# Kernel optimization log

Measured on AMD Instinct MI355X. Metric: run time of the kernel, lower is better.

Reference implementation:

```python
import jax, jax.numpy as jnp
import numpy as np

# ---- neuron / simulation params (network.yaml analogue) ----
THETA = 10.0      # spike threshold
TAU_SR = 4.0      # SRM (psp) kernel time constant
TAU_REF = 4.0     # refractory kernel time constant
SCALE_REF = 2.0
TS = 1.0          # simulation step
T_SAMPLE = 1000
N_BATCH, N_IN, N_OUT = 16, 2048, 512
SPIKE_RATE = 0.1


def _alpha_kernel(tau, mult, eps_cut):
    # SLAYER _calculateAlphaKernel: truncated alpha function samples
    vals = []
    for t in np.arange(0.0, T_SAMPLE, TS):
        v = mult * t / tau * np.exp(1.0 - t / tau)
        if abs(v) < eps_cut and t > tau:
            break
        vals.append(v)
    return np.asarray(vals, dtype=np.float32)

SRM_KERNEL = _alpha_kernel(TAU_SR, 1.0, 0.01)
REF_KERNEL = _alpha_kernel(TAU_REF, -SCALE_REF * THETA, 0.0001)  # fullRefKernel=True
# pending-refractory shift vector: refKernel[0]==0 is consumed at spike time
REF_SHIFT = jnp.asarray(np.concatenate([REF_KERNEL[1:], [0.0]]).astype(np.float32))


def psp(spike_in):
    # causal temporal filter: psp[n,c,t] = Ts * sum_j srm[j] * s[n,c,t-j]
    N, C, T = spike_in.shape
    Ls = SRM_KERNEL.shape[0]
    x = spike_in.reshape(N * C, 1, T)
    k = jnp.asarray(SRM_KERNEL)[::-1].reshape(1, 1, Ls)  # flip -> convolution
    y = jax.lax.conv_general_dilated(
        x, k, window_strides=(1,), padding=[(Ls - 1, 0)],
        dimension_numbers=('NCH', 'OIH', 'NCH'))
    return y.reshape(N, C, T) * TS


def spike_scan(wpsp):
    # sequential spike generation with refractory feedback (SLAYER getSpikes)
    N, C, T = wpsp.shape
    L = REF_SHIFT.shape[0]

    def step(buf, x):
        u = x + buf[..., 0]                       # membrane incl. past refractory
        ind = (u >= THETA).astype(x.dtype)
        buf = jnp.concatenate([buf[..., 1:], jnp.zeros_like(buf[..., :1])], -1) \
              + ind[..., None] * REF_SHIFT        # schedule refractory for future t
        return buf, (ind / TS, u)

    buf0 = jnp.zeros((N, C, L), wpsp.dtype)
    _, (s, u) = jax.lax.scan(step, buf0, jnp.moveaxis(wpsp, -1, 0))
    return jnp.moveaxis(s, 0, -1), jnp.moveaxis(u, 0, -1)


def setup_inputs() -> dict:
    key = jax.random.key(0)
    k1, k2 = jax.random.split(key)
    spikeInput = (jax.random.uniform(k1, (N_BATCH, N_IN, T_SAMPLE)) < SPIKE_RATE
                  ).astype(jnp.float32)
    weight = jax.random.normal(k2, (N_OUT, N_IN), dtype=jnp.float32) * 0.3
    return {'spikeInput': spikeInput, 'weight': weight}


def reference(spikeInput, weight):
    p = psp(spikeInput)                           # [N, Nin, T]
    wpsp = jnp.einsum('oi,nit->not', weight, p)   # 1x1x1 conv == matmul, no bias
    spikes, _ = spike_scan(wpsp)                  # [N, Nout, T]
    return spikes
```

## Files before the change

kernel.cpp:

```cpp
#include <hip/hip_runtime.h>
#include <hip/hip_bf16.h>
#include <math.h>

#define NB 16
#define NIN 2048
#define NOUT 512
#define TT 1000
#define L_SRM 31

typedef int v4i  __attribute__((ext_vector_type(4)));
typedef int v16i __attribute__((ext_vector_type(16)));

__device__ __forceinline__ unsigned long long spread8(unsigned int b) {
    unsigned long long x = (unsigned long long)(b & 0xFFu) * 0x0101010101010101ULL;
    x &= 0x8040201008040201ULL;
    x |= x >> 4; x |= x >> 2; x |= x >> 1;
    return x & 0x0101010101010101ULL;
}

__global__ __launch_bounds__(256) void k_quant(const float* __restrict__ W,
                                               signed char* __restrict__ Bq) {
    int idx = blockIdx.x * 256 + threadIdx.x;
    int o = idx >> 11, i = idx & (NIN - 1);
    double w = (double)W[o * NIN + i];
    int wq = (int)rint(w * 536870912.0);
    int b0 = (int)(signed char)(wq & 255); int r = (wq - b0) >> 8;
    int b1 = (int)(signed char)(r  & 255); r = (r - b1) >> 8;
    int b2 = (int)(signed char)(r  & 255); r = (r - b2) >> 8;
    int b3 = r;
    size_t e = (size_t)o * NIN + i;
    Bq[e]                = (signed char)b0;
    Bq[e + 1048576]      = (signed char)b1;
    Bq[e + 2097152]      = (signed char)b2;
    Bq[e + 3145728]      = (signed char)b3;
}

__global__ __launch_bounds__(256) void k_extract(const float* __restrict__ s,
                                                 unsigned long long* __restrict__ bits) {
    __shared__ float tile[64][65];
    int tc = blockIdx.x, ic = blockIdx.y, n = blockIdx.z;
    int t0 = tc * 64, i0 = ic * 64;
    int tid = threadIdx.x;
    int r = tid >> 2, cq = tid & 3;
    const float* rp = s + ((size_t)(n * NIN + i0 + r)) * TT + t0;
    #pragma unroll
    for (int q = 0; q < 4; ++q) {
        int col = cq * 16 + q * 4;
        float4 v = make_float4(0.f, 0.f, 0.f, 0.f);
        if (t0 + col + 3 < TT) v = *(const float4*)(rp + col);
        tile[r][col] = v.x; tile[r][col + 1] = v.y;
        tile[r][col + 2] = v.z; tile[r][col + 3] = v.w;
    }
    __syncthreads();
    int lane = tid & 63, w = tid >> 6;
    #pragma unroll
    for (int k = 0; k < 16; ++k) {
        int tl = w * 16 + k;
        if (t0 + tl >= TT) break;
        unsigned long long m = __ballot(tile[lane][tl] != 0.0f);
        if (lane == 0) bits[((size_t)n * TT + t0 + tl) * 32 + ic] = m;
    }
}

__global__ __launch_bounds__(512) void k_spmm(const unsigned long long* __restrict__ bits,
                                              const signed char* __restrict__ Bq,
                                              double* __restrict__ z) {
    __shared__ char Alds[128 * 128];
    __shared__ char Blds[4][64 * 128];
    int tid = threadIdx.x;
    int bid = blockIdx.x;
    int o0  = (bid & 7) * 64;
    int nt0 = (bid >> 3) * 128;

    const int arow_w = tid >> 2, q = tid & 3;
    const int p_st = tid >> 7, orow = (tid >> 1) & 63, h = tid & 1;
    const unsigned int* agp = (const unsigned int*)bits + (size_t)(nt0 + arow_w) * 64 + q;
    const signed char*  bgp = Bq + (size_t)p_st * (NOUT * NIN)
                                 + (size_t)(o0 + orow) * NIN + h * 64;
    char* awp = Alds + arow_w * 128;
    const int xra_w = arow_w & 7;
    char* bwp = Blds[p_st] + orow * 128;
    const int xro_w = orow & 7;

    const int l = tid & 63, wv = tid >> 6;
    const int wm = wv >> 1, wn = wv & 1;
    const int arow = wm * 32 + (l & 31), xra = arow & 7;
    const int brow = wn * 32 + (l & 31), xrb = brow & 7;
    const int kg = l >> 5;

    v16i acc0 = {}, acc1 = {}, acc2 = {}, acc3 = {};

    unsigned int aw = agp[0];
    int4 bs0 = ((const int4*)bgp)[0], bs1 = ((const int4*)bgp)[1],
         bs2 = ((const int4*)bgp)[2], bs3 = ((const int4*)bgp)[3];

    for (int ks = 0; ks < 16; ++ks) {
        __syncthreads();
        {
            unsigned long long s0 = spread8(aw), s1 = spread8(aw >> 8),
                               s2 = spread8(aw >> 16), s3 = spread8(aw >> 24);
            ulonglong2 v0; v0.x = s0; v0.y = s1;
            ulonglong2 v1; v1.x = s2; v1.y = s3;
            *(ulonglong2*)(awp + (((2 * q)     ^ xra_w) << 4)) = v0;
            *(ulonglong2*)(awp + (((2 * q + 1) ^ xra_w) << 4)) = v1;
            *(int4*)(bwp + (((h * 4 + 0) ^ xro_w) << 4)) = bs0;
            *(int4*)(bwp + (((h * 4 + 1) ^ xro_w) << 4)) = bs1;
            *(int4*)(bwp + (((h * 4 + 2) ^ xro_w) << 4)) = bs2;
            *(int4*)(bwp + (((h * 4 + 3) ^ xro_w) << 4)) = bs3;
        }
        __syncthreads();
        if (ks < 15) {
            aw = agp[(ks + 1) * 4];
            const int4* g = (const int4*)(bgp + (size_t)(ks + 1) * 128);
            bs0 = g[0]; bs1 = g[1]; bs2 = g[2]; bs3 = g[3];
        }
        #pragma unroll
        for (int ksub = 0; ksub < 4; ++ksub) {
            int ca = ksub * 2 + kg;
            v4i av  = *(const v4i*)(Alds    + arow * 128 + (((ca) ^ xra) << 4));
            v4i bv0 = *(const v4i*)(Blds[0] + brow * 128 + (((ca) ^ xrb) << 4));
            v4i bv1 = *(const v4i*)(Blds[1] + brow * 128 + (((ca) ^ xrb) << 4));
            v4i bv2 = *(const v4i*)(Blds[2] + brow * 128 + (((ca) ^ xrb) << 4));
            v4i bv3 = *(const v4i*)(Blds[3] + brow * 128 + (((ca) ^ xrb) << 4));
            acc0 = __builtin_amdgcn_mfma_i32_32x32x32_i8(av, bv0, acc0, 0, 0, 0);
            acc1 = __builtin_amdgcn_mfma_i32_32x32x32_i8(av, bv1, acc1, 0, 0, 0);
            acc2 = __builtin_amdgcn_mfma_i32_32x32x32_i8(av, bv2, acc2, 0, 0, 0);
            acc3 = __builtin_amdgcn_mfma_i32_32x32x32_i8(av, bv3, acc3, 0, 0, 0);
        }
    }

    #pragma unroll
    for (int r = 0; r < 16; ++r) {
        int row = (r & 3) + 8 * (r >> 2) + 4 * kg;
        long long tot = ((long long)acc3[r] << 24) + ((long long)acc2[r] << 16)
                      + ((long long)acc1[r] << 8)  +  (long long)acc0[r];
        double zv = (double)tot * (1.0 / 536870912.0);
        __builtin_nontemporal_store(zv,
            &z[(size_t)(nt0 + wm * 32 + row) * NOUT + (o0 + wn * 32 + (l & 31))]);
    }
}

__global__ __launch_bounds__(128) void k_conv(const double* __restrict__ z,
                                              double* __restrict__ wpsp) {
    __shared__ float srm_s[32];
    __shared__ __align__(16) double zs[62 * 128];
    int tid = threadIdx.x;
    if (tid < L_SRM) {
        double t = (double)tid;
        srm_s[tid] = (float)((t / 4.0) * exp(1.0 - t / 4.0));
    }
    int tb = blockIdx.x * 32;
    int oc = blockIdx.y * 128;
    int n  = blockIdx.z;
    const double* zp = z + ((size_t)n * TT) * NOUT + oc;
    int wv = tid >> 6, lane = tid & 63;
    for (int r = wv; r < 62; r += 2) {
        int t = tb - 30 + r;
        if (t >= 0 && t < TT) {
            const double* src = zp + (size_t)t * NOUT + lane * 2;
            __builtin_amdgcn_global_load_lds(
                (const __attribute__((address_space(1))) void*)src,
                (__attribute__((address_space(3))) void*)(&zs[r * 128]),
                16, 0, 0);
        } else {
            double2 zero; zero.x = 0.0; zero.y = 0.0;
            *(double2*)(&zs[r * 128 + lane * 2]) = zero;
        }
    }
    asm volatile("s_waitcnt vmcnt(0)" ::: "memory");
    __syncthreads();
    for (int tl = 0; tl < 32; ++tl) {
        int t = tb + tl;
        if (t >= TT) break;
        double a0 = 0., a1 = 0., a2 = 0., a3 = 0.;
        #pragma unroll
        for (int jj = 0; jj < 28; jj += 4) {
            a0 += (double)srm_s[jj]     * zs[(tl + 30 - jj) * 128 + tid];
            a1 += (double)srm_s[jj + 1] * zs[(tl + 29 - jj) * 128 + tid];
            a2 += (double)srm_s[jj + 2] * zs[(tl + 28 - jj) * 128 + tid];
            a3 += (double)srm_s[jj + 3] * zs[(tl + 27 - jj) * 128 + tid];
        }
        a0 += (double)srm_s[28] * zs[(tl + 2) * 128 + tid];
        a1 += (double)srm_s[29] * zs[(tl + 1) * 128 + tid];
        a2 += (double)srm_s[30] * zs[(tl + 0) * 128 + tid];
        wpsp[((size_t)n * TT + t) * NOUT + oc + tid] = (a0 + a1) + (a2 + a3);
    }
}

__global__ __launch_bounds__(64) void k_scan(const double* __restrict__ wpsp,
                                             float* __restrict__ out) {
    __shared__ float  refTab[64];
    __shared__ double Tb[8][256];
    __shared__ __align__(16) double xbuf[2][34 * 64];
    __shared__ float  obuf[64 * 33];
    int lane = threadIdx.x;
    {
        double d = (double)lane;
        refTab[lane] = (lane == 0) ? 0.0f
                     : (float)(-20.0 * (d / 4.0) * exp(1.0 - d / 4.0));
    }
    __syncthreads();
    for (int e = lane; e < 2048; e += 64) {
        int k = e >> 8, m = e & 255;
        double s = 0.0;
        #pragma unroll
        for (int j = 0; j < 8; ++j) {
            int idx = 8 * k + j + 1;
            if (((m >> j) & 1) && idx <= 63) s += (double)refTab[idx];
        }
        Tb[k][m] = s;
    }

    int n  = blockIdx.x >> 3;
    int o0 = (blockIdx.x & 7) << 6;
    const double* wp = wpsp + ((size_t)n * TT) * NOUT + o0;
    float* op = out + ((size_t)(n * NOUT) + o0 + lane) * TT;
    const double* Tb0 = &Tb[0][0];

    int halfSel = lane >> 5;
    int colSel  = (lane & 31) * 2;
    #define STAGE(bf, tb, nrows)                                                   \
        for (int p = 0; p < (nrows) / 2; ++p) {                                    \
            const double* src = wp + (size_t)((tb) + 2 * p + halfSel) * NOUT + colSel; \
            __builtin_amdgcn_global_load_lds(                                      \
                (const __attribute__((address_space(1))) void*)src,                \
                (__attribute__((address_space(3))) void*)(&xbuf[bf][p * 128]),     \
                16, 0, 0);                                                         \
        }

    int buf = 0;
    STAGE(0, 0, 32);
    asm volatile("s_waitcnt vmcnt(0)" ::: "memory");
    __syncthreads();

    unsigned long long h = 0ULL;
    bool sp1 = false;
    double xp = xbuf[0][lane];
    double x1 = xbuf[0][64 + lane];
    double partial1 = 0.0;
    double p0 = 0., p1 = 0., p2 = 0., p3 = 0., p4 = 0., p5 = 0., p6 = 0.;
    double e0 = 0.0, e1 = 0.0;
    double c1_0 = Tb0[0], c1_1 = Tb0[1], c1_2 = Tb0[2], c1_3 = Tb0[3];

    for (int tb = 0; tb < TT; tb += 32) {
        int nnext = TT - (tb + 32); if (nnext > 32) nnext = 32;
        if (nnext > 0) { STAGE(buf ^ 1, tb + 32, nnext); }
        #pragma unroll
        for (int tl = 0; tl < 32; ++tl) {
            h = (h << 1) | (unsigned long long)sp1;
            unsigned long long hs = h << 2;
            double q1 = Tb[1][(unsigned)((hs >>  8) & 255)];
            double q2 = Tb[2][(unsigned)((hs >> 16) & 255)];
            double q3 = Tb[3][(unsigned)((hs >> 24) & 255)];
            double q4 = Tb[4][(unsigned)((hs >> 32) & 255)];
            double q5 = Tb[5][(unsigned)((hs >> 40) & 255)];
            double q6 = Tb[6][(unsigned)((hs >> 48) & 255)];
            double q7 = Tb[7][(unsigned)((hs >> 56) & 255)];
            unsigned m = (unsigned)(hs & 255);
            double2 nc01 = *(const double2*)(Tb0 + m);
            double2 nc23 = *(const double2*)(Tb0 + m + 2);
            double nx = xbuf[buf][(tl + 2) * 64 + lane];
            double e0n = sp1 ? c1_2 : c1_0;
            double e1n = sp1 ? c1_3 : c1_1;
            double np1 = ((p0 + p1) + (p2 + p3)) + ((p4 + p5) + p6);
            double u = xp + (sp1 ? e1 : e0);
            bool spt = (u >= 10.0);
            obuf[lane * 33 + tl] = spt ? 1.0f : 0.0f;
            double nxp = x1 + np1;
            sp1 = spt;
            e0 = e0n; e1 = e1n;
            partial1 = np1;
            xp = nxp; x1 = nx;
            p0 = q1; p1 = q2; p2 = q3; p3 = q4; p4 = q5; p5 = q6; p6 = q7;
            c1_0 = nc01.x; c1_1 = nc01.y; c1_2 = nc23.x; c1_3 = nc23.y;
        }
        int nrows = TT - tb; if (nrows > 32) nrows = 32;
        for (int k = 0; k + 3 < nrows; k += 4) {
            float4 v = make_float4(obuf[lane * 33 + k],     obuf[lane * 33 + k + 1],
                                   obuf[lane * 33 + k + 2], obuf[lane * 33 + k + 3]);
            *(float4*)(op + tb + k) = v;
        }
        asm volatile("s_waitcnt vmcnt(0)" ::: "memory");
        __syncthreads();
        buf ^= 1;
        xp = xbuf[buf][lane] + partial1;
        x1 = xbuf[buf][64 + lane];
    }
    #undef STAGE
}

extern "C" void kernel_launch(void* const* d_in, const int* in_sizes, int n_in,
                              void* d_out, int out_size, void* d_ws, size_t ws_size,
                              hipStream_t stream) {
    const float* spikeInput = (const float*)d_in[0];
    const float* weight     = (const float*)d_in[1];
    float* out = (float*)d_out;

    char* ws = (char*)d_ws;
    unsigned long long* bits = (unsigned long long*)ws;
    signed char*        Bq   = (signed char*)(ws + 4194304);
    double*             z    = (double*)(ws + 8388608);
    double*             wpsp = (double*)(ws + 73924608);

    k_quant<<<(NOUT * NIN) / 256, 256, 0, stream>>>(weight, Bq);
    k_extract<<<dim3(16, 32, 16), 256, 0, stream>>>(spikeInput, bits);
    k_spmm<<<1000, 512, 0, stream>>>(bits, Bq, z);
    k_conv<<<dim3(32, 4, 16), 128, 0, stream>>>(z, wpsp);
    k_scan<<<128, 64, 0, stream>>>(wpsp, out);
}
```

Before: 481.7 us.

## Split scan refractory table lookups across two half-waves per output column

New measurement: 513.0 us. +6.5%, slower.

```diff
diff --git a/kernel.cpp b/kernel.cpp
--- a/kernel.cpp
+++ b/kernel.cpp
@@ -191,8 +191,8 @@
                                              float* __restrict__ out) {
     __shared__ float  refTab[64];
     __shared__ double Tb[8][256];
-    __shared__ __align__(16) double xbuf[2][34 * 64];
-    __shared__ float  obuf[64 * 33];
+    __shared__ __align__(16) double xbuf[2][34 * 32];
+    __shared__ float  obuf[32 * 33];
     int lane = threadIdx.x;
     {
         double d = (double)lane;
@@ -211,17 +211,20 @@
         Tb[k][m] = s;
     }
 
-    int n  = blockIdx.x >> 3;
-    int o0 = (blockIdx.x & 7) << 6;
+    int n  = blockIdx.x >> 4;
+    int o0 = (blockIdx.x & 15) << 5;
+    int ol = lane & 31;
+    int g  = lane >> 5;
     const double* wp = wpsp + ((size_t)n * TT) * NOUT + o0;
-    float* op = out + ((size_t)(n * NOUT) + o0 + lane) * TT;
+    float* op = out + ((size_t)(n * NOUT) + o0 + ol) * TT;
     const double* Tb0 = &Tb[0][0];
-
-    int halfSel = lane >> 5;
-    int colSel  = (lane & 31) * 2;
+    const int kA = 1 + 3 * g, kB = 2 + 3 * g, kC = 3 + 3 * g;
+    const int shA = 8 + 24 * g, shB = 16 + 24 * g, shC = 24 + 24 * g;
+
     #define STAGE(bf, tb, nrows)                                                   \
-        for (int p = 0; p < (nrows) / 2; ++p) {                                    \
-            const double* src = wp + (size_t)((tb) + 2 * p + halfSel) * NOUT + colSel; \
+        for (int p = 0; p < (nrows) / 4; ++p) {                                    \
+            const double* src = wp + (size_t)((tb) + 4 * p + (lane >> 4)) * NOUT   \
+                                   + (lane & 15) * 2;                              \
             __builtin_amdgcn_global_load_lds(                                      \
                 (const __attribute__((address_space(1))) void*)src,                \
                 (__attribute__((address_space(3))) void*)(&xbuf[bf][p * 128]),     \
@@ -235,10 +238,10 @@
 
     unsigned long long h = 0ULL;
     bool sp1 = false;
-    double xp = xbuf[0][lane];
-    double x1 = xbuf[0][64 + lane];
+    double xp = xbuf[0][ol];
+    double x1 = xbuf[0][32 + ol];
     double partial1 = 0.0;
-    double p0 = 0., p1 = 0., p2 = 0., p3 = 0., p4 = 0., p5 = 0., p6 = 0.;
+    double pA = 0., pB = 0., pC = 0., pE = 0.;
     double e0 = 0.0, e1 = 0.0;
     double c1_0 = Tb0[0], c1_1 = Tb0[1], c1_2 = Tb0[2], c1_3 = Tb0[3];
 
@@ -249,42 +252,40 @@
         for (int tl = 0; tl < 32; ++tl) {
             h = (h << 1) | (unsigned long long)sp1;
             unsigned long long hs = h << 2;
-            double q1 = Tb[1][(unsigned)((hs >>  8) & 255)];
-            double q2 = Tb[2][(unsigned)((hs >> 16) & 255)];
-            double q3 = Tb[3][(unsigned)((hs >> 24) & 255)];
-            double q4 = Tb[4][(unsigned)((hs >> 32) & 255)];
-            double q5 = Tb[5][(unsigned)((hs >> 40) & 255)];
-            double q6 = Tb[6][(unsigned)((hs >> 48) & 255)];
-            double q7 = Tb[7][(unsigned)((hs >> 56) & 255)];
+            double tA = Tb[kA][(unsigned)((hs >> shA) & 255)];
+            double tB = Tb[kB][(unsigned)((hs >> shB) & 255)];
+            double tC = Tb[kC][(unsigned)((hs >> shC) & 255)];
+            double tE = Tb[7][(unsigned)((hs >> 56) & 255)];
+            double nx = xbuf[buf][(tl + 2) * 32 + ol];
             unsigned m = (unsigned)(hs & 255);
             double2 nc01 = *(const double2*)(Tb0 + m);
             double2 nc23 = *(const double2*)(Tb0 + m + 2);
-            double nx = xbuf[buf][(tl + 2) * 64 + lane];
             double e0n = sp1 ? c1_2 : c1_0;
             double e1n = sp1 ? c1_3 : c1_1;
-            double np1 = ((p0 + p1) + (p2 + p3)) + ((p4 + p5) + p6);
+            double loc = (pA + pB) + (pC + (g ? 0.0 : pE));
+            double np1 = loc + __shfl_xor(loc, 32);
             double u = xp + (sp1 ? e1 : e0);
             bool spt = (u >= 10.0);
-            obuf[lane * 33 + tl] = spt ? 1.0f : 0.0f;
+            if (g == 0) obuf[ol * 33 + tl] = spt ? 1.0f : 0.0f;
             double nxp = x1 + np1;
-            sp1 = spt;
-            e0 = e0n; e1 = e1n;
-            partial1 = np1;
+            sp1 = spt; e0 = e0n; e1 = e1n; partial1 = np1;
             xp = nxp; x1 = nx;
-            p0 = q1; p1 = q2; p2 = q3; p3 = q4; p4 = q5; p5 = q6; p6 = q7;
+            pA = tA; pB = tB; pC = tC; pE = tE;
             c1_0 = nc01.x; c1_1 = nc01.y; c1_2 = nc23.x; c1_3 = nc23.y;
         }
         int nrows = TT - tb; if (nrows > 32) nrows = 32;
-        for (int k = 0; k + 3 < nrows; k += 4) {
-            float4 v = make_float4(obuf[lane * 33 + k],     obuf[lane * 33 + k + 1],
-                                   obuf[lane * 33 + k + 2], obuf[lane * 33 + k + 3]);
-            *(float4*)(op + tb + k) = v;
+        if (g == 0) {
+            for (int k = 0; k + 3 < nrows; k += 4) {
+                float4 v = make_float4(obuf[ol * 33 + k],     obuf[ol * 33 + k + 1],
+                                       obuf[ol * 33 + k + 2], obuf[ol * 33 + k + 3]);
+                *(float4*)(op + tb + k) = v;
+            }
         }
         asm volatile("s_waitcnt vmcnt(0)" ::: "memory");
         __syncthreads();
         buf ^= 1;
-        xp = xbuf[buf][lane] + partial1;
-        x1 = xbuf[buf][64 + lane];
+        xp = xbuf[buf][ol] + partial1;
+        x1 = xbuf[buf][32 + ol];
     }
     #undef STAGE
 }
@@ -306,5 +307,5 @@
     k_extract<<<dim3(16, 32, 16), 256, 0, stream>>>(spikeInput, bits);
     k_spmm<<<1000, 512, 0, stream>>>(bits, Bq, z);
     k_conv<<<dim3(32, 4, 16), 128, 0, stream>>>(z, wpsp);
-    k_scan<<<128, 64, 0, stream>>>(wpsp, out);
-}
+    k_scan<<<256, 64, 0, stream>>>(wpsp, out);
+}
```

## Replace LDS double-buffered staging in scan with register prefetch queue

Applied to the files above, without the earlier changes.

After: 482.2 us. Within noise of the previous version (+0.1%).

```diff
diff --git a/kernel.cpp b/kernel.cpp
--- a/kernel.cpp
+++ b/kernel.cpp
@@ -191,8 +191,6 @@
                                              float* __restrict__ out) {
     __shared__ float  refTab[64];
     __shared__ double Tb[8][256];
-    __shared__ __align__(16) double xbuf[2][34 * 64];
-    __shared__ float  obuf[64 * 33];
     int lane = threadIdx.x;
     {
         double d = (double)lane;
@@ -210,43 +208,31 @@
         }
         Tb[k][m] = s;
     }
+    __syncthreads();
 
     int n  = blockIdx.x >> 3;
     int o0 = (blockIdx.x & 7) << 6;
-    const double* wp = wpsp + ((size_t)n * TT) * NOUT + o0;
+    const double* xsrc = wpsp + ((size_t)n * TT) * NOUT + o0 + lane;
     float* op = out + ((size_t)(n * NOUT) + o0 + lane) * TT;
     const double* Tb0 = &Tb[0][0];
 
-    int halfSel = lane >> 5;
-    int colSel  = (lane & 31) * 2;
-    #define STAGE(bf, tb, nrows)                                                   \
-        for (int p = 0; p < (nrows) / 2; ++p) {                                    \
-            const double* src = wp + (size_t)((tb) + 2 * p + halfSel) * NOUT + colSel; \
-            __builtin_amdgcn_global_load_lds(                                      \
-                (const __attribute__((address_space(1))) void*)src,                \
-                (__attribute__((address_space(3))) void*)(&xbuf[bf][p * 128]),     \
-                16, 0, 0);                                                         \
-        }
-
-    int buf = 0;
-    STAGE(0, 0, 32);
-    asm volatile("s_waitcnt vmcnt(0)" ::: "memory");
-    __syncthreads();
+    double xp = xsrc[0];
+    double x1 = xsrc[NOUT];
+    double xq[8];
+    #pragma unroll
+    for (int j = 0; j < 8; ++j) xq[(j + 2) & 7] = xsrc[(size_t)(j + 2) * NOUT];
 
     unsigned long long h = 0ULL;
     bool sp1 = false;
-    double xp = xbuf[0][lane];
-    double x1 = xbuf[0][64 + lane];
-    double partial1 = 0.0;
     double p0 = 0., p1 = 0., p2 = 0., p3 = 0., p4 = 0., p5 = 0., p6 = 0.;
     double e0 = 0.0, e1 = 0.0;
     double c1_0 = Tb0[0], c1_1 = Tb0[1], c1_2 = Tb0[2], c1_3 = Tb0[3];
 
-    for (int tb = 0; tb < TT; tb += 32) {
-        int nnext = TT - (tb + 32); if (nnext > 32) nnext = 32;
-        if (nnext > 0) { STAGE(buf ^ 1, tb + 32, nnext); }
-        #pragma unroll
-        for (int tl = 0; tl < 32; ++tl) {
+    for (int tb = 0; tb < TT; tb += 8) {
+        unsigned omask = 0;
+        #pragma unroll
+        for (int tl = 0; tl < 8; ++tl) {
+            int t = tb + tl;
             h = (h << 1) | (unsigned long long)sp1;
             unsigned long long hs = h << 2;
             double q1 = Tb[1][(unsigned)((hs >>  8) & 255)];
@@ -259,34 +245,29 @@
             unsigned m = (unsigned)(hs & 255);
             double2 nc01 = *(const double2*)(Tb0 + m);
             double2 nc23 = *(const double2*)(Tb0 + m + 2);
-            double nx = xbuf[buf][(tl + 2) * 64 + lane];
+            double nx = xq[(tl + 2) & 7];
+            int tload = t + 10; if (tload > TT - 1) tload = TT - 1;
+            xq[(tl + 2) & 7] = xsrc[(size_t)tload * NOUT];
             double e0n = sp1 ? c1_2 : c1_0;
             double e1n = sp1 ? c1_3 : c1_1;
             double np1 = ((p0 + p1) + (p2 + p3)) + ((p4 + p5) + p6);
             double u = xp + (sp1 ? e1 : e0);
             bool spt = (u >= 10.0);
-            obuf[lane * 33 + tl] = spt ? 1.0f : 0.0f;
+            omask |= ((unsigned)spt) << tl;
             double nxp = x1 + np1;
-            sp1 = spt;
-            e0 = e0n; e1 = e1n;
-            partial1 = np1;
+            sp1 = spt; e0 = e0n; e1 = e1n;
             xp = nxp; x1 = nx;
             p0 = q1; p1 = q2; p2 = q3; p3 = q4; p4 = q5; p5 = q6; p6 = q7;
             c1_0 = nc01.x; c1_1 = nc01.y; c1_2 = nc23.x; c1_3 = nc23.y;
         }
-        int nrows = TT - tb; if (nrows > 32) nrows = 32;
-        for (int k = 0; k + 3 < nrows; k += 4) {
-            float4 v = make_float4(obuf[lane * 33 + k],     obuf[lane * 33 + k + 1],
-                                   obuf[lane * 33 + k + 2], obuf[lane * 33 + k + 3]);
-            *(float4*)(op + tb + k) = v;
-        }
-        asm volatile("s_waitcnt vmcnt(0)" ::: "memory");
-        __syncthreads();
-        buf ^= 1;
-        xp = xbuf[buf][lane] + partial1;
-        x1 = xbuf[buf][64 + lane];
-    }
-    #undef STAGE
+        float4 v0, v1;
+        v0.x = (omask & 1u)   ? 1.0f : 0.0f;  v0.y = (omask & 2u)   ? 1.0f : 0.0f;
+        v0.z = (omask & 4u)   ? 1.0f : 0.0f;  v0.w = (omask & 8u)   ? 1.0f : 0.0f;
+        v1.x = (omask & 16u)  ? 1.0f : 0.0f;  v1.y = (omask & 32u)  ? 1.0f : 0.0f;
+        v1.z = (omask & 64u)  ? 1.0f : 0.0f;  v1.w = (omask & 128u) ? 1.0f : 0.0f;
+        *(float4*)(op + tb)     = v0;
+        *(float4*)(op + tb + 4) = v1;
+    }
 }
 
 extern "C" void kernel_launch(void* const* d_in, const int* in_sizes, int n_in,
```
